# Kernel tuning notes

Measured on AMD Instinct MI355X. Metric: run time of the kernel, lower is better.

Reference implementation:

```python
import jax, jax.numpy as jnp
import numpy as np

B, S, D, H = 2, 2048, 2048, 16
HD = D // H  # 128
THETA = 10000.0


def _rope_cos_sin(seq_len, head_dim):
    # matches LlamaRotaryEmbedding: inv_freq = 1/theta^(2i/d), emb = cat(freqs, freqs)
    inv_freq = 1.0 / (THETA ** (jnp.arange(0, head_dim, 2, dtype=jnp.float32) / head_dim))
    t = jnp.arange(seq_len, dtype=jnp.float32)
    freqs = jnp.einsum('s,d->sd', t, inv_freq)          # [S, HD/2]
    emb = jnp.concatenate([freqs, freqs], axis=-1)       # [S, HD]
    return jnp.cos(emb), jnp.sin(emb)


def _rotate_half(x):
    x1, x2 = jnp.split(x, 2, axis=-1)
    return jnp.concatenate([-x2, x1], axis=-1)


def setup_inputs() -> dict:
    key = jax.random.key(0)
    ks = jax.random.split(key, 5)
    scale = D ** -0.5
    x = jax.random.normal(ks[0], (B, S, D), jnp.float32)
    wq = jax.random.normal(ks[1], (D, D), jnp.float32) * scale
    wk = jax.random.normal(ks[2], (D, D), jnp.float32) * scale
    wv = jax.random.normal(ks[3], (D, D), jnp.float32) * scale
    wo = jax.random.normal(ks[4], (D, D), jnp.float32) * scale
    # additive causal mask (0 on/below diagonal, large negative above)
    causal = jnp.tril(jnp.ones((S, S), dtype=bool))
    mask = jnp.where(causal, 0.0, -1e9).astype(jnp.float32)[None, None]  # [1,1,S,S]
    return {"x": x, "wq": wq, "wk": wk, "wv": wv, "wo": wo, "mask": mask}


def reference(x, wq, wk, wv, wo, mask):
    b, s, d = x.shape
    # projections + head split: [b, H, s, HD]
    q = (x @ wq).reshape(b, s, H, HD).transpose(0, 2, 1, 3)
    k = (x @ wk).reshape(b, s, H, HD).transpose(0, 2, 1, 3)
    v = (x @ wv).reshape(b, s, H, HD).transpose(0, 2, 1, 3)
    # inline RoPE on q and k (positions 0..s-1 along the seq axis)
    cos, sin = _rope_cos_sin(s, HD)
    cos = cos[None, None]  # [1,1,s,HD]
    sin = sin[None, None]
    q = q * cos + _rotate_half(q) * sin
    k = k * cos + _rotate_half(k) * sin
    # eager attention: QK^T * scale + mask -> softmax -> @ V
    attn = jnp.einsum('bhqd,bhkd->bhqk', q, k) * (HD ** -0.5)
    attn = jax.nn.softmax(attn + mask, axis=-1)
    out = jnp.einsum('bhqk,bhkd->bhqd', attn, v)
    out = out.transpose(0, 2, 1, 3).reshape(b, s, d)
    return out @ wo
```

## Files before the change

### kernel.cpp

```cpp
#include <hip/hip_runtime.h>

#define S_LEN 2048
#define D_DIM 2048
#define NH 16
#define HD 128
#define NB 2
#define NROW (NB * S_LEN)
#define QKV_STR 6144

typedef unsigned short bf16;
typedef __attribute__((ext_vector_type(8))) short bf16x8;
typedef __attribute__((ext_vector_type(4))) float f32x4;
typedef __attribute__((ext_vector_type(16))) float f32x16;
typedef __attribute__((address_space(3))) unsigned int as3u;
typedef __attribute__((address_space(1))) unsigned int as1u;

__device__ __forceinline__ void gload16(const void* g, void* l) {
  __builtin_amdgcn_global_load_lds((const as1u*)g, (as3u*)l, 16, 0, 0);
}

__device__ __forceinline__ unsigned short f2bf(float f) {
  unsigned u = __builtin_bit_cast(unsigned, f);
  u += 0x7FFFu + ((u >> 16) & 1u);
  return (unsigned short)(u >> 16);
}
__device__ __forceinline__ float bf2f(unsigned short b) {
  return __builtin_bit_cast(float, (unsigned)b << 16);
}
__device__ __forceinline__ unsigned cvtpk(float lo, float hi) {
  unsigned r;
  asm("v_cvt_pk_bf16_f32 %0, %1, %2" : "=v"(r) : "v"(lo), "v"(hi));
  return r;
}
__device__ __forceinline__ float exp2a(float x) {
  float r;
  asm("v_exp_f32 %0, %1" : "=v"(r) : "v"(x));
  return r;
}


__global__ void rope_table_k(float2* __restrict__ tab) {
  int i = blockIdx.x * 256 + threadIdx.x;
  int s = i >> 6, d = i & 63;
  float invf = powf(10000.0f, -(float)d * (1.0f / 64.0f));
  float ang = (float)s * invf;
  tab[i] = make_float2(cosf(ang), sinf(ang));
}

__global__ void convert_x_k(const float* __restrict__ src, bf16* __restrict__ dst) {
  int i = (blockIdx.x * 256 + threadIdx.x) * 4;
  float4 v = *(const float4*)(src + i);
  ushort4 w;
  w.x = f2bf(v.x); w.y = f2bf(v.y); w.z = f2bf(v.z); w.w = f2bf(v.w);
  *(ushort4*)(dst + i) = w;
}

__global__ void transpose_w_k(const float* __restrict__ W, bf16* __restrict__ Wt) {
  __shared__ float t[64][65];
  int c0 = blockIdx.x * 64, r0 = blockIdx.y * 64;
  int tx = threadIdx.x & 63, ty = threadIdx.x >> 6;
#pragma unroll
  for (int i = 0; i < 16; ++i)
    t[ty + i * 4][tx] = W[(size_t)(r0 + ty + i * 4) * D_DIM + c0 + tx];
  __syncthreads();
#pragma unroll
  for (int i = 0; i < 16; ++i)
    Wt[(size_t)(c0 + ty + i * 4) * D_DIM + r0 + tx] = f2bf(t[tx][ty + i * 4]);
}

__global__ void transpose_v_k(const bf16* __restrict__ Vsrc, bf16* __restrict__ Vt) {
  __shared__ bf16 t[64][65];
  int bh = blockIdx.z;
  int b = bh >> 4, h = bh & 15;
  int s0 = blockIdx.x * 64, d0 = blockIdx.y * 64;
  int tx = threadIdx.x & 63, ty = threadIdx.x >> 6;
  const bf16* src = Vsrc + (size_t)(b * S_LEN + s0) * QKV_STR + h * HD + d0;
#pragma unroll
  for (int i = 0; i < 16; ++i)
    t[ty + i * 4][tx] = src[(size_t)(ty + i * 4) * QKV_STR + tx];
  __syncthreads();
  bf16* dst = Vt + ((size_t)bh * HD + d0) * S_LEN + s0;
#pragma unroll
  for (int i = 0; i < 16; ++i)
    dst[(size_t)(ty + i * 4) * S_LEN + tx] = t[tx][ty + i * 4];
}

__global__ void rope_apply_k(bf16* __restrict__ qkv, const float2* __restrict__ tab) {
  int i = blockIdx.x * 256 + threadIdx.x;
  int d = i & 63;
  int t = i >> 6;
  int h = t & 15;
  int row = t >> 4;
  int s = row & (S_LEN - 1);
  const float qscale = 0.12751743f;
  float2 cs = tab[s * 64 + d];
  size_t base = (size_t)row * QKV_STR + h * HD + d;
  float x1 = bf2f(qkv[base]), x2 = bf2f(qkv[base + 64]);
  qkv[base]      = f2bf((x1 * cs.x - x2 * cs.y) * qscale);
  qkv[base + 64] = f2bf((x2 * cs.x + x1 * cs.y) * qscale);
  size_t kb2 = base + 2048;
  float y1 = bf2f(qkv[kb2]), y2 = bf2f(qkv[kb2 + 64]);
  qkv[kb2]      = f2bf(y1 * cs.x - y2 * cs.y);
  qkv[kb2 + 64] = f2bf(y2 * cs.x + y1 * cs.y);
}


__device__ __forceinline__ void storec(bf16* p, float v) { *p = f2bf(v); }
__device__ __forceinline__ void storec(float* p, float v) { *p = v; }

template <typename OutT>
__global__ __launch_bounds__(256) void gemm_bt_k(
    const bf16* __restrict__ A, const bf16* __restrict__ Bt,
    OutT* __restrict__ C, int M, int N, int K) {
  __shared__ bf16 As[128 * 32];
  __shared__ bf16 Bs[128 * 32];
  const int tid = threadIdx.x;
  const int lane = tid & 63;
  const int wid = tid >> 6;
  const int bm = blockIdx.y * 128;
  const int bn = blockIdx.x * 128;
  const int wr = (wid >> 1) * 64;
  const int wc = (wid & 1) * 64;
  const int lr = lane & 15;
  const int kg = lane >> 4;

  f32x4 acc[4][4] = {};

  const int c0 = wid * 2;
  const int srow = lane >> 2;
  const int scol = (lane & 3) * 8;
  const bf16* Ap0 = A + (size_t)(bm + c0 * 16 + srow) * K + scol;
  const bf16* Ap1 = Ap0 + (size_t)16 * K;
  const bf16* Bp0 = Bt + (size_t)(bn + c0 * 16 + srow) * K + scol;
  const bf16* Bp1 = Bp0 + (size_t)16 * K;
  bf16* Asd0 = &As[c0 * 512];
  bf16* Asd1 = &As[(c0 + 1) * 512];
  bf16* Bsd0 = &Bs[c0 * 512];
  bf16* Bsd1 = &Bs[(c0 + 1) * 512];

  for (int k0 = 0; k0 < K; k0 += 32) {
    __syncthreads();
    gload16(Ap0 + k0, Asd0);
    gload16(Ap1 + k0, Asd1);
    gload16(Bp0 + k0, Bsd0);
    gload16(Bp1 + k0, Bsd1);
    __syncthreads();
    bf16x8 a[4], b[4];
#pragma unroll
    for (int m = 0; m < 4; ++m)
      a[m] = *(const bf16x8*)&As[(wr + m * 16 + lr) * 32 + kg * 8];
#pragma unroll
    for (int n = 0; n < 4; ++n)
      b[n] = *(const bf16x8*)&Bs[(wc + n * 16 + lr) * 32 + kg * 8];
#pragma unroll
    for (int m = 0; m < 4; ++m)
#pragma unroll
      for (int n = 0; n < 4; ++n)
        acc[m][n] = __builtin_amdgcn_mfma_f32_16x16x32_bf16(a[m], b[n], acc[m][n], 0, 0, 0);
  }

#pragma unroll
  for (int m = 0; m < 4; ++m) {
    int row0 = bm + wr + m * 16 + kg * 4;
#pragma unroll
    for (int n = 0; n < 4; ++n) {
      int col = bn + wc + n * 16 + lr;
#pragma unroll
      for (int r = 0; r < 4; ++r)
        storec(&C[(size_t)(row0 + r) * N + col], acc[m][n][r]);
    }
  }
}


#define PH_READ_A(DST, FB, P)                                                  \
  _Pragma("unroll") for (int mm = 0; mm < 4; ++mm)                             \
    _Pragma("unroll") for (int ks = 0; ks < 2; ++ks)                           \
      DST[mm][ks] = *(const bf16x8*)&smem[(P)*16384 + wm * 8192 +              \
                                          (((FB) + mm) * 2 + ks) * 512 + lane * 8];
#define PH_READ_B(DST, NFB, P)                                                 \
  _Pragma("unroll") for (int j = 0; j < 2; ++j)                                \
    _Pragma("unroll") for (int ks = 0; ks < 2; ++ks)                           \
      DST[j][ks] = *(const bf16x8*)&smem[32768 + (P)*16384 + hb * 8192 +       \
                                         ((wn1 * 4 + (NFB) + j) * 2 + ks) * 512 + lane * 8];
#define STAGE_A(KT, H, P)                                                      \
  { int k0_ = ((KT) & 31) * 64;                                                \
    gload16(Apt + (H)*262144 + k0_, &smem[(P)*16384 + (H)*8192 + w * 512]);    \
    gload16(Apt + (H)*262144 + 131072 + k0_,                                   \
            &smem[(P)*16384 + (H)*8192 + (8 + w) * 512]); }
#define STAGE_B(KT, H, P)                                                      \
  { int k0_ = ((KT) & 31) * 64;                                                \
    gload16(Bpt + (H)*262144 + k0_, &smem[32768 + (P)*16384 + (H)*8192 + w * 512]); \
    gload16(Bpt + (H)*262144 + 131072 + k0_,                                   \
            &smem[32768 + (P)*16384 + (H)*8192 + (8 + w) * 512]); }
#define MFMA_Q(AF, BF, MB, NB)                                                 \
  _Pragma("unroll") for (int mm = 0; mm < 4; ++mm)                             \
    _Pragma("unroll") for (int j = 0; j < 2; ++j)                              \
      _Pragma("unroll") for (int ks = 0; ks < 2; ++ks)                         \
        acc[(MB) + mm][(NB) + j] = __builtin_amdgcn_mfma_f32_16x16x32_bf16(    \
            AF[mm][ks], BF[j][ks], acc[(MB) + mm][(NB) + j], 0, 0, 0);
#define PH_TAIL                                                                \
  __builtin_amdgcn_s_barrier();                                                \
  asm volatile("s_waitcnt lgkmcnt(0)" ::: "memory");                           \
  __builtin_amdgcn_sched_barrier(0);                                           \
  __builtin_amdgcn_s_setprio(1);
#define PH_END                                                                 \
  __builtin_amdgcn_s_setprio(0);                                               \
  __builtin_amdgcn_s_barrier();

#define GROUP(KT, P)                                                           \
  {                                                                            \
    bf16x8 a0[4][2], a1[4][2], b0[2][2], b1[2][2];                             \
                                                       \
    PH_READ_A(a0, 0, P); PH_READ_B(b0, 0, P);                                  \
    STAGE_B((KT) + 1, 1, (P) ^ 1);                                             \
    PH_TAIL                                                                    \
    MFMA_Q(a0, b0, 0, 0);                                                      \
    PH_END                                                                     \
                                                       \
    PH_READ_A(a1, 4, P);                                                       \
    PH_TAIL                                                                    \
    MFMA_Q(a1, b0, 4, 0);                                                      \
    PH_END                                                                     \
                                                       \
    PH_READ_B(b1, 2, P);                                                       \
    STAGE_A((KT) + 2, 0, P); STAGE_A((KT) + 2, 1, P);                          \
    PH_TAIL                                                                    \
    MFMA_Q(a1, b1, 4, 2);                                                      \
    PH_END                                                                     \
                                                       \
    STAGE_B((KT) + 2, 0, P);                                                   \
    PH_TAIL                                                                    \
    MFMA_Q(a0, b1, 0, 2);                                                      \
    __builtin_amdgcn_s_setprio(0);                                             \
    asm volatile("s_waitcnt vmcnt(6)" ::: "memory");                           \
    __builtin_amdgcn_sched_barrier(0);                                         \
    __builtin_amdgcn_s_barrier();                                              \
  }

__global__ __launch_bounds__(512, 2) void gemm256_k(
    const bf16* __restrict__ A, const bf16* __restrict__ Bt,
    bf16* __restrict__ C, int N) {
  __shared__ bf16 smem[65536];
  const int tid = threadIdx.x;
  const int lane = tid & 63;
  const int w = tid >> 6;
  const int wm = w >> 2;
  const int wn = w & 3;
  const int wn1 = wn & 1;
  const int hb = wn >> 1;
  const int bm = blockIdx.y * 256;
  const int bn = blockIdx.x * 256;

  const bf16* Apt = A + (size_t)(bm + (w >> 1) * 16 + (lane & 15)) * 2048 +
                    (w & 1) * 32 + (lane >> 4) * 8;
  const bf16* Bpt = Bt + (size_t)(bn + (w >> 1) * 16 + (lane & 15)) * 2048 +
                    (w & 1) * 32 + (lane >> 4) * 8;

  f32x4 acc[8][4] = {};

  STAGE_A(0, 0, 0); STAGE_A(0, 1, 0); STAGE_B(0, 0, 0); STAGE_B(0, 1, 0);
  STAGE_A(1, 0, 1); STAGE_A(1, 1, 1); STAGE_B(1, 0, 1);
  asm volatile("s_waitcnt vmcnt(6)" ::: "memory");
  __builtin_amdgcn_sched_barrier(0);
  __builtin_amdgcn_s_barrier();

  for (int t = 0; t < 32; t += 2) {
    GROUP(t, 0);
    GROUP(t + 1, 1);
  }

#pragma unroll
  for (int mF = 0; mF < 8; ++mF) {
    int row0 = bm + wm * 128 + mF * 16 + (lane >> 4) * 4;
#pragma unroll
    for (int nf = 0; nf < 4; ++nf) {
      int col = bn + wn * 64 + nf * 16 + (lane & 15);
#pragma unroll
      for (int r = 0; r < 4; ++r)
        C[(size_t)(row0 + r) * N + col] = f2bf(acc[mF][nf][r]);
    }
  }
}

#define FBODY(T, CUR0, CUR1, NXT0, NXT1)                                         \
  {                                                                              \
    const int kv0_ = (T) * 64;                                                   \
    stageV(kv0_ + 64, ((T) + 1) & 1);                                            \
    stageK(kv0_ + 128, (T) & 1);                                                 \
    if (kv0_ + 64 <= qw0 + 31) {                                                 \
      NXT0 = 0.0f; NXT1 = 0.0f;                                                  \
      const bf16* krow0_ = &sh[(((T) + 1) & 1) * 8192] + (size_t)l31 * 128;      \
      const bf16* krow1_ = krow0_ + 32 * 128;                                    \
      _Pragma("unroll")                                                          \
      for (int ks = 0; ks < 8; ++ks) {                                           \
        int cb_ = ((ks * 32) ^ kxor) >> 1;                                       \
        bf16x8 kf0_ = *(const bf16x8*)(krow0_ + cb_);                            \
        bf16x8 kf1_ = *(const bf16x8*)(krow1_ + cb_);                            \
        NXT0 = __builtin_amdgcn_mfma_f32_32x32x16_bf16(kf0_, qf[ks], NXT0, 0, 0, 0); \
        NXT1 = __builtin_amdgcn_mfma_f32_32x32x16_bf16(kf1_, qf[ks], NXT1, 0, 0, 0); \
      }                                                                          \
    }                                                                            \
    if (kv0_ <= qw0 + 31) {                                                      \
      if (kv0_ + 63 > qw0) {                                                     \
        _Pragma("unroll")                                                        \
        for (int r = 0; r < 16; ++r) {                                           \
          int kvg_ = kv0_ + (r & 3) + 8 * (r >> 2) + 4 * h;                      \
          if (kvg_ > q) CUR0[r] = -3.0e38f;                                      \
          if (kvg_ + 32 > q) CUR1[r] = -3.0e38f;                                 \
        }                                                                        \
      }                                                                          \
      float tm_[8];                                                              \
      _Pragma("unroll")                                                          \
      for (int r = 0; r < 8; ++r)                                                \
        tm_[r] = fmaxf(fmaxf(CUR0[r], CUR0[r + 8]), fmaxf(CUR1[r], CUR1[r + 8])); \
      _Pragma("unroll")                                                          \
      for (int r = 0; r < 4; ++r) tm_[r] = fmaxf(tm_[r], tm_[r + 4]);            \
      float mt_ = fmaxf(fmaxf(tm_[0], tm_[1]), fmaxf(tm_[2], tm_[3]));           \
      mt_ = fmaxf(mt_, __shfl_xor(mt_, 32));                                     \
      if (__any(mt_ > m_run + 8.0f)) {                                           \
        float mnew_ = fmaxf(m_run, mt_);                                         \
        float alpha_ = exp2a(m_run - mnew_);                                     \
        l_run *= alpha_;                                                         \
        _Pragma("unroll")                                                        \
        for (int n = 0; n < 4; ++n)                                              \
          _Pragma("unroll")                                                      \
          for (int r = 0; r < 16; ++r) ot[n][r] *= alpha_;                       \
        m_run = mnew_;                                                           \
      }                                                                          \
      float rs_[16];                                                             \
      _Pragma("unroll")                                                          \
      for (int r = 0; r < 16; ++r) {                                             \
        CUR0[r] = exp2a(CUR0[r] - m_run);                                        \
        CUR1[r] = exp2a(CUR1[r] - m_run);                                        \
        rs_[r] = CUR0[r] + CUR1[r];                                              \
      }                                                                          \
      _Pragma("unroll")                                                          \
      for (int r = 0; r < 8; ++r) rs_[r] += rs_[r + 8];                          \
      _Pragma("unroll")                                                          \
      for (int r = 0; r < 4; ++r) rs_[r] += rs_[r + 4];                          \
      float rsum_ = (rs_[0] + rs_[1]) + (rs_[2] + rs_[3]);                       \
      rsum_ += __shfl_xor(rsum_, 32);                                            \
      l_run += rsum_;                                                            \
      unsigned wd0_[8], wd1_[8];                                                 \
      _Pragma("unroll")                                                          \
      for (int j = 0; j < 8; ++j) {                                              \
        wd0_[j] = cvtpk(CUR0[2 * j], CUR0[2 * j + 1]);                           \
        wd1_[j] = cvtpk(CUR1[2 * j], CUR1[2 * j + 1]);                           \
      }                                                                          \
      const bf16* Vbuf_ = &sh[16384 + ((T) & 1) * 8192];                         \
      _Pragma("unroll")                                                          \
      for (int t4 = 0; t4 < 4; ++t4) {                                           \
        const unsigned* wdp_ = (t4 >> 1) ? wd1_ : wd0_;                          \
        int a0_ = 4 * (t4 & 1) + 2 * h;                                          \
        int sidx_ = 4 * (t4 & 1) + 2 * (1 - h);                                  \
        unsigned s0_ = (unsigned)__shfl_xor((int)wdp_[sidx_], 32);               \
        unsigned s1_ = (unsigned)__shfl_xor((int)wdp_[sidx_ + 1], 32);           \
        unsigned pb4_[4];                                                        \
        pb4_[0] = h ? s0_ : wdp_[a0_];                                           \
        pb4_[1] = h ? s1_ : wdp_[a0_ + 1];                                       \
        pb4_[2] = h ? wdp_[a0_] : s0_;                                           \
        pb4_[3] = h ? wdp_[a0_ + 1] : s1_;                                       \
        bf16x8 pb_ = __builtin_bit_cast(bf16x8, *(uint4*)pb4_);                  \
        int cb_ = ((t4 * 32) ^ vxor) >> 1;                                       \
        _Pragma("unroll")                                                        \
        for (int n = 0; n < 4; ++n) {                                            \
          bf16x8 va_ = *(const bf16x8*)(Vbuf_ + (size_t)(32 * n + l31) * 64 + cb_); \
          ot[n] = __builtin_amdgcn_mfma_f32_32x32x16_bf16(va_, pb_, ot[n], 0, 0, 0); \
        }                                                                        \
      }                                                                          \
    }                                                                            \
    asm volatile("s_waitcnt vmcnt(0)" ::: "memory");                             \
    __builtin_amdgcn_s_barrier();                                                \
    __builtin_amdgcn_sched_barrier(0);                                           \
  }

__global__ __launch_bounds__(256, 2) void flash_attn_k(
    const bf16* __restrict__ Q, const bf16* __restrict__ Kb,
    const bf16* __restrict__ Vt, bf16* __restrict__ O) {
  __shared__ bf16 sh[32768];
  const int tid = threadIdx.x;
  const int lane = tid & 63;
  const int w = tid >> 6;
  const int h = lane >> 5;
  const int l31 = lane & 31;
  const int bh = blockIdx.y;
  const int b = bh >> 4;
  const int hh = bh & 15;
  const int qb = (gridDim.x - 1 - blockIdx.x) * 128;
  const int qw0 = qb + 32 * w;
  const int q = qw0 + l31;

  const bf16* qp = Q + (size_t)(b * S_LEN + q) * QKV_STR + hh * HD + h * 8;
  bf16x8 qf[8];
#pragma unroll
  for (int ks = 0; ks < 8; ++ks) qf[ks] = *(const bf16x8*)(qp + ks * 16);

  f32x16 ot[4] = {};
  float m_run = -3.0e38f, l_run = 0.f;

  const bf16* Kg = Kb + (size_t)(b * S_LEN) * QKV_STR + hh * HD;
  const bf16* Vg = Vt + (size_t)bh * HD * S_LEN;

  const int kst_row = 16 * w + (lane >> 4);
  const int vst_row = 32 * w + (lane >> 3);
  const int vst_col = (((lane & 7) ^ (lane >> 3)) << 3);
  const int kxor = (16 * h) ^ ((l31 & 15) << 4);
  const int vxor = (16 * h) ^ ((l31 & 7) << 4);

  auto stageK = [&](int kv0, int buf) {
#pragma unroll
    for (int jj = 0; jj < 4; ++jj) {
      int kr = (kv0 + kst_row + jj * 4) & (S_LEN - 1);
      gload16(Kg + (size_t)kr * QKV_STR + (((lane & 15) ^ (jj * 4 + (lane >> 4))) << 3),
              &sh[buf * 8192 + (16 * w + jj * 4) * 128]);
    }
  };
  auto stageV = [&](int kv0, int buf) {
    int c = (kv0 & (S_LEN - 1)) + vst_col;
#pragma unroll
    for (int jj = 0; jj < 4; ++jj) {
      int vr = vst_row + jj * 8;
      gload16(Vg + (size_t)vr * S_LEN + c, &sh[16384 + buf * 8192 + (32 * w + jj * 8) * 64]);
    }
  };

  stageK(0, 0);
  stageV(0, 0);
  stageK(64, 1);
  asm volatile("s_waitcnt vmcnt(8)" ::: "memory");
  __builtin_amdgcn_s_barrier();
  __builtin_amdgcn_sched_barrier(0);

  f32x16 stA0 = 0.0f, stA1 = 0.0f, stB0, stB1;
  {
    const bf16* krow0 = &sh[0] + (size_t)l31 * 128;
    const bf16* krow1 = krow0 + 32 * 128;
#pragma unroll
    for (int ks = 0; ks < 8; ++ks) {
      int cb = ((ks * 32) ^ kxor) >> 1;
      bf16x8 kf0 = *(const bf16x8*)(krow0 + cb);
      bf16x8 kf1 = *(const bf16x8*)(krow1 + cb);
      stA0 = __builtin_amdgcn_mfma_f32_32x32x16_bf16(kf0, qf[ks], stA0, 0, 0, 0);
      stA1 = __builtin_amdgcn_mfma_f32_32x32x16_bf16(kf1, qf[ks], stA1, 0, 0, 0);
    }
  }
  asm volatile("s_waitcnt vmcnt(0)" ::: "memory");
  __builtin_amdgcn_s_barrier();
  __builtin_amdgcn_sched_barrier(0);

  const int nt = qb / 64 + 2;
  int t = 0;
  for (; t + 1 < nt; t += 2) {
    FBODY(t, stA0, stA1, stB0, stB1);
    FBODY(t + 1, stB0, stB1, stA0, stA1);
  }
  if (t < nt) FBODY(t, stA0, stA1, stB0, stB1);

  float inv = 1.0f / l_run;
  bf16* ow = &sh[w * 4096];
#pragma unroll
  for (int n = 0; n < 4; ++n)
#pragma unroll
    for (int rq = 0; rq < 4; ++rq) {
      int dbase = 32 * n + 8 * rq + 4 * h;
      unsigned u0 = cvtpk(ot[n][4 * rq + 0] * inv, ot[n][4 * rq + 1] * inv);
      unsigned u1 = cvtpk(ot[n][4 * rq + 2] * inv, ot[n][4 * rq + 3] * inv);
      uint2 uu = make_uint2(u0, u1);
      *(uint2*)(ow + l31 * 128 + (dbase ^ ((l31 & 15) << 3))) = uu;
    }
  __syncthreads();
#pragma unroll
  for (int p = 0; p < 8; ++p) {
    int qr = p * 4 + (lane >> 4);
    int ce = ((((lane & 15) << 4) ^ ((qr & 15) << 4)) >> 1);
    bf16x8 vrow = *(const bf16x8*)(ow + qr * 128 + ce);
    *(bf16x8*)(O + (size_t)(b * S_LEN + qw0 + qr) * D_DIM + hh * HD + (lane & 15) * 8) = vrow;
  }
}


extern "C" void kernel_launch(void* const* d_in, const int* in_sizes, int n_in,
                              void* d_out, int out_size, void* d_ws, size_t ws_size,
                              hipStream_t stream) {
  (void)in_sizes; (void)n_in; (void)out_size; (void)ws_size;
  const float* x  = (const float*)d_in[0];
  const float* wq = (const float*)d_in[1];
  const float* wk = (const float*)d_in[2];
  const float* wv = (const float*)d_in[3];
  const float* wo = (const float*)d_in[4];
  float* out = (float*)d_out;

  char* ws = (char*)d_ws;
  const size_t MB = 1u << 20;
  bf16* xb    = (bf16*)(ws + 0 * MB);
  bf16* Ob    = xb;
  bf16* wTall = (bf16*)(ws + 16 * MB);
  bf16* wTo   = (bf16*)(ws + 40 * MB);
  bf16* QKV   = (bf16*)(ws + 48 * MB);
  bf16* Vtb   = (bf16*)(ws + 96 * MB);
  float2* tab = (float2*)(ws + 112 * MB);

  rope_table_k<<<512, 256, 0, stream>>>(tab);
  convert_x_k<<<8192, 256, 0, stream>>>(x, xb);
  dim3 tg(32, 32);
  transpose_w_k<<<tg, 256, 0, stream>>>(wq, wTall);
  transpose_w_k<<<tg, 256, 0, stream>>>(wk, wTall + (size_t)2048 * D_DIM);
  transpose_w_k<<<tg, 256, 0, stream>>>(wv, wTall + (size_t)4096 * D_DIM);
  transpose_w_k<<<tg, 256, 0, stream>>>(wo, wTo);

  gemm256_k<<<dim3(QKV_STR / 256, NROW / 256), 512, 0, stream>>>(
      xb, wTall, QKV, QKV_STR);

  rope_apply_k<<<16384, 256, 0, stream>>>(QKV, tab);
  transpose_v_k<<<dim3(32, 2, 32), 256, 0, stream>>>(QKV + 4096, Vtb);

  flash_attn_k<<<dim3(S_LEN / 128, NB * NH), 256, 0, stream>>>(
      QKV, QKV + 2048, Vtb, Ob);

  gemm_bt_k<float><<<dim3(D_DIM / 128, NROW / 128), 256, 0, stream>>>(
      Ob, wTo, out, NROW, D_DIM, D_DIM);
}
```

Measured before the change: 353.9 us.

## Deepen K prefetch to triple buffer and respread GEMM global loads across phases

The flash attention kernel now keeps K in three LDS buffers and prefetches two tiles ahead. The per-iteration wait drops from vmcnt(0) to vmcnt(4), so the next V/K loads can stay in flight across the barrier. The GEMM main loop redistributes its A/B staging loads more evenly over the four MFMA phases, with a partial lgkmcnt wait and a relaxed vmcnt. The attention kernel uses more LDS (80KB per block), which may cut occupancy at 2 blocks per CU, and the looser waits add ordering risk.

Result: no change. 353.8 us (-0.0%).

```diff
diff --git a/kernel.cpp b/kernel.cpp
--- a/kernel.cpp
+++ b/kernel.cpp
@@ -199,41 +199,44 @@
       _Pragma("unroll") for (int ks = 0; ks < 2; ++ks)                         \
         acc[(MB) + mm][(NB) + j] = __builtin_amdgcn_mfma_f32_16x16x32_bf16(    \
             AF[mm][ks], BF[j][ks], acc[(MB) + mm][(NB) + j], 0, 0, 0);
-#define PH_TAIL                                                                \
+#define PH_MID                                                                 \
   __builtin_amdgcn_s_barrier();                                                \
   asm volatile("s_waitcnt lgkmcnt(0)" ::: "memory");                           \
   __builtin_amdgcn_sched_barrier(0);                                           \
   __builtin_amdgcn_s_setprio(1);
-#define PH_END                                                                 \
+#define PH_CLOSE                                                               \
   __builtin_amdgcn_s_setprio(0);                                               \
   __builtin_amdgcn_s_barrier();
 
 #define GROUP(KT, P)                                                           \
   {                                                                            \
     bf16x8 a0[4][2], a1[4][2], b0[2][2], b1[2][2];                             \
-                                                       \
+                                 \
     PH_READ_A(a0, 0, P); PH_READ_B(b0, 0, P);                                  \
+    STAGE_B((KT) + 1, 0, (P) ^ 1);                                             \
+    asm volatile("s_waitcnt lgkmcnt(8)" ::: "memory");                         \
+    PH_MID                                                                     \
+    MFMA_Q(a0, b0, 0, 0);                                                      \
+    PH_CLOSE                                                                   \
+                                  \
+    PH_READ_A(a1, 4, P);                                                       \
     STAGE_B((KT) + 1, 1, (P) ^ 1);                                             \
-    PH_TAIL                                                                    \
-    MFMA_Q(a0, b0, 0, 0);                                                      \
-    PH_END                                                                     \
-                                                       \
-    PH_READ_A(a1, 4, P);                                                       \
-    PH_TAIL                                                                    \
+    PH_MID                                                                     \
     MFMA_Q(a1, b0, 4, 0);                                                      \
-    PH_END                                                                     \
-                                                       \
+    PH_CLOSE                                                                   \
+                                  \
     PH_READ_B(b1, 2, P);                                                       \
-    STAGE_A((KT) + 2, 0, P); STAGE_A((KT) + 2, 1, P);                          \
-    PH_TAIL                                                                    \
+    STAGE_A((KT) + 2, 0, P);                                                   \
+    PH_MID                                                                     \
     MFMA_Q(a1, b1, 4, 2);                                                      \
-    PH_END                                                                     \
-                                                       \
-    STAGE_B((KT) + 2, 0, P);                                                   \
-    PH_TAIL                                                                    \
+    PH_CLOSE                                                                   \
+                            \
+    STAGE_A((KT) + 2, 1, P);                                                   \
+    __builtin_amdgcn_s_barrier();                                              \
+    __builtin_amdgcn_s_setprio(1);                                             \
     MFMA_Q(a0, b1, 0, 2);                                                      \
     __builtin_amdgcn_s_setprio(0);                                             \
-    asm volatile("s_waitcnt vmcnt(6)" ::: "memory");                           \
+    asm volatile("s_waitcnt vmcnt(4)" ::: "memory");                           \
     __builtin_amdgcn_sched_barrier(0);                                         \
     __builtin_amdgcn_s_barrier();                                              \
   }
@@ -260,8 +263,8 @@
   f32x4 acc[8][4] = {};
 
   STAGE_A(0, 0, 0); STAGE_A(0, 1, 0); STAGE_B(0, 0, 0); STAGE_B(0, 1, 0);
-  STAGE_A(1, 0, 1); STAGE_A(1, 1, 1); STAGE_B(1, 0, 1);
-  asm volatile("s_waitcnt vmcnt(6)" ::: "memory");
+  STAGE_A(1, 0, 1); STAGE_A(1, 1, 1);
+  asm volatile("s_waitcnt vmcnt(4)" ::: "memory");
   __builtin_amdgcn_sched_barrier(0);
   __builtin_amdgcn_s_barrier();
 
@@ -269,6 +272,9 @@
     GROUP(t, 0);
     GROUP(t + 1, 1);
   }
+
+  asm volatile("s_waitcnt vmcnt(0)" ::: "memory");
+  __builtin_amdgcn_s_barrier();
 
 #pragma unroll
   for (int mF = 0; mF < 8; ++mF) {
@@ -287,10 +293,11 @@
   {                                                                              \
     const int kv0_ = (T) * 64;                                                   \
     stageV(kv0_ + 64, ((T) + 1) & 1);                                            \
-    stageK(kv0_ + 128, (T) & 1);                                                 \
+    stageK(kv0_ + 192, kb_st);                                                   \
+    kb_st = (kb_st == 2) ? 0 : kb_st + 1;                                        \
     if (kv0_ + 64 <= qw0 + 31) {                                                 \
       NXT0 = 0.0f; NXT1 = 0.0f;                                                  \
-      const bf16* krow0_ = &sh[(((T) + 1) & 1) * 8192] + (size_t)l31 * 128;      \
+      const bf16* krow0_ = &sh[kb_rd * 8192] + (size_t)l31 * 128;                \
       const bf16* krow1_ = krow0_ + 32 * 128;                                    \
       _Pragma("unroll")                                                          \
       for (int ks = 0; ks < 8; ++ks) {                                           \
@@ -301,6 +308,7 @@
         NXT1 = __builtin_amdgcn_mfma_f32_32x32x16_bf16(kf1_, qf[ks], NXT1, 0, 0, 0); \
       }                                                                          \
     }                                                                            \
+    kb_rd = (kb_rd == 2) ? 0 : kb_rd + 1;                                        \
     if (kv0_ <= qw0 + 31) {                                                      \
       if (kv0_ + 63 > qw0) {                                                     \
         _Pragma("unroll")                                                        \
@@ -348,7 +356,7 @@
         wd0_[j] = cvtpk(CUR0[2 * j], CUR0[2 * j + 1]);                           \
         wd1_[j] = cvtpk(CUR1[2 * j], CUR1[2 * j + 1]);                           \
       }                                                                          \
-      const bf16* Vbuf_ = &sh[16384 + ((T) & 1) * 8192];                         \
+      const bf16* Vbuf_ = &sh[24576 + ((T) & 1) * 8192];                         \
       _Pragma("unroll")                                                          \
       for (int t4 = 0; t4 < 4; ++t4) {                                           \
         const unsigned* wdp_ = (t4 >> 1) ? wd1_ : wd0_;                          \
@@ -370,15 +378,15 @@
         }                                                                        \
       }                                                                          \
     }                                                                            \
-    asm volatile("s_waitcnt vmcnt(0)" ::: "memory");                             \
+    asm volatile("s_waitcnt vmcnt(4)" ::: "memory");                             \
+    __builtin_amdgcn_sched_barrier(0);                                           \
     __builtin_amdgcn_s_barrier();                                                \
-    __builtin_amdgcn_sched_barrier(0);                                           \
   }
 
 __global__ __launch_bounds__(256, 2) void flash_attn_k(
     const bf16* __restrict__ Q, const bf16* __restrict__ Kb,
     const bf16* __restrict__ Vt, bf16* __restrict__ O) {
-  __shared__ bf16 sh[32768];
+  __shared__ bf16 sh[40960];
   const int tid = threadIdx.x;
   const int lane = tid & 63;
   const int w = tid >> 6;
@@ -421,16 +429,17 @@
 #pragma unroll
     for (int jj = 0; jj < 4; ++jj) {
       int vr = vst_row + jj * 8;
-      gload16(Vg + (size_t)vr * S_LEN + c, &sh[16384 + buf * 8192 + (32 * w + jj * 8) * 64]);
+      gload16(Vg + (size_t)vr * S_LEN + c, &sh[24576 + buf * 8192 + (32 * w + jj * 8) * 64]);
     }
   };
 
   stageK(0, 0);
   stageV(0, 0);
   stageK(64, 1);
-  asm volatile("s_waitcnt vmcnt(8)" ::: "memory");
+  stageK(128, 2);
+  asm volatile("s_waitcnt vmcnt(12)" ::: "memory");
+  __builtin_amdgcn_sched_barrier(0);
   __builtin_amdgcn_s_barrier();
-  __builtin_amdgcn_sched_barrier(0);
 
   f32x16 stA0 = 0.0f, stA1 = 0.0f, stB0, stB1;
   {
@@ -445,10 +454,12 @@
       stA1 = __builtin_amdgcn_mfma_f32_32x32x16_bf16(kf1, qf[ks], stA1, 0, 0, 0);
     }
   }
-  asm volatile("s_waitcnt vmcnt(0)" ::: "memory");
+  asm volatile("s_waitcnt vmcnt(4)" ::: "memory");
+  __builtin_amdgcn_sched_barrier(0);
   __builtin_amdgcn_s_barrier();
-  __builtin_amdgcn_sched_barrier(0);
-
+
+  int kb_st = 0;
+  int kb_rd = 1;
   const int nt = qb / 64 + 2;
   int t = 0;
   for (; t + 1 < nt; t += 2) {
@@ -456,6 +467,9 @@
     FBODY(t + 1, stB0, stB1, stA0, stA1);
   }
   if (t < nt) FBODY(t, stA0, stA1, stB0, stB1);
+
+  asm volatile("s_waitcnt vmcnt(0)" ::: "memory");
+  __builtin_amdgcn_s_barrier();
 
   float inv = 1.0f / l_run;
   bf16* ow = &sh[w * 4096];
```
